# Kernel tuning notes

Measured on AMD Instinct MI355X. Metric: run time of the kernel, lower is better.

The kernel has to match this reference:

```python
import jax, jax.numpy as jnp
import numpy as np

B, H, V, T = 2048, 512, 64, 128

def setup_inputs() -> dict:
    key = jax.random.key(0)
    ks = jax.random.split(key, 7)
    s = 1.0 / np.sqrt(H)
    return {
        "z": jax.random.normal(ks[0], (B, H), dtype=jnp.float32),
        "w_ih": jax.random.uniform(ks[1], (4 * H, H), jnp.float32, -s, s),
        "w_hh": jax.random.uniform(ks[2], (4 * H, H), jnp.float32, -s, s),
        "b_ih": jax.random.uniform(ks[3], (4 * H,), jnp.float32, -s, s),
        "b_hh": jax.random.uniform(ks[4], (4 * H,), jnp.float32, -s, s),
        "fc_w": jax.random.uniform(ks[5], (V, H), jnp.float32, -s, s),
        "fc_b": jax.random.uniform(ks[6], (V,), jnp.float32, -s, s),
    }

def reference(z, w_ih, w_hh, b_ih, b_hh, fc_w, fc_b):
    batch = z.shape[0]
    # Input z is identical at every timestep -> precompute its gate contribution once.
    x_gates = z @ w_ih.T + b_ih + b_hh  # [B, 4H]

    def step(carry, _):
        h, c = carry
        gates = x_gates + h @ w_hh.T  # [B, 4H]
        i, f, g, o = jnp.split(gates, 4, axis=-1)  # PyTorch LSTMCell gate order
        i = jax.nn.sigmoid(i)
        f = jax.nn.sigmoid(f)
        g = jnp.tanh(g)
        o = jax.nn.sigmoid(o)
        c = f * c + i * g
        h = o * jnp.tanh(c)
        return (h, c), h

    h0 = jnp.zeros((batch, w_hh.shape[1]), dtype=z.dtype)
    c0 = jnp.zeros_like(h0)
    _, hs = jax.lax.scan(step, (h0, c0), None, length=T)  # [T, B, H]
    x = jnp.transpose(hs, (1, 0, 2))  # [B, T, H]
    return jax.nn.relu(x @ fc_w.T + fc_b)  # [B, T, V]
```

## Files before the change

kernel.cpp:

```cpp
#include <hip/hip_runtime.h>
#include <hip/hip_bf16.h>
#include <cstdint>

#define B_   2048
#define H_   512
#define T_   128
#define V_   64
#define FOURH 2048

typedef __bf16 bf16x8 __attribute__((ext_vector_type(8)));
typedef float  floatx4 __attribute__((ext_vector_type(4)));
typedef int    intx4   __attribute__((ext_vector_type(4)));

__device__ __forceinline__ unsigned short f2bf(float f) {
    union { float f; uint32_t u; } v; v.f = f;
    uint32_t r = v.u + 0x7fff + ((v.u >> 16) & 1);
    return (unsigned short)(r >> 16);
}

__device__ __forceinline__ float rcp_(float x) {
    float r; asm("v_rcp_f32 %0, %1" : "=v"(r) : "v"(x)); return r;
}
__device__ __forceinline__ float sigmoidf_(float x) {
    return rcp_(1.0f + __expf(-x));
}
__device__ __forceinline__ float tanhf_(float x) {
    float e = __expf(fminf(-2.0f * x, 80.0f));
    return (1.0f - e) * rcp_(1.0f + e);
}

__device__ __forceinline__ void global_to_lds16(const unsigned short* g, unsigned short* l) {
    __builtin_amdgcn_global_load_lds(
        (const __attribute__((address_space(1))) unsigned int*)g,
        (__attribute__((address_space(3))) unsigned int*)l, 16, 0, 0);
}

__device__ __forceinline__ bf16x8 load16_sys(const unsigned short* p) {
    bf16x8 d;
    asm volatile("global_load_dwordx4 %0, %1, off sc0 sc1\n\t"
                 "s_waitcnt vmcnt(0)"
                 : "=v"(d) : "v"(p));
    return d;
}

__device__ __forceinline__ void flag_prefetch(const unsigned int* fp, intx4& f) {
    asm volatile("global_load_dwordx4 %0, %1, off sc0 sc1"
                 : "=v"(f) : "v"(fp) : "memory");
}
__device__ __forceinline__ bool flag_ok(const intx4& f, unsigned int tgt) {
    return (unsigned int)f[0] >= tgt && (unsigned int)f[1] >= tgt &&
           (unsigned int)f[2] >= tgt && (unsigned int)f[3] >= tgt;
}
__device__ __forceinline__ void wait4(const unsigned int* fp, unsigned int tgt) {
    for (;;) {
        intx4 f;
        asm volatile("global_load_dwordx4 %0, %1, off sc0 sc1\n\t"
                     "s_waitcnt vmcnt(0)"
                     : "=v"(f) : "v"(fp) : "memory");
        if (flag_ok(f, tgt)) return;
        __builtin_amdgcn_s_sleep(1);
    }
}
__device__ __forceinline__ void flag_post(unsigned int* p, unsigned int v) {
    asm volatile("global_store_dword %0, %1, off sc0 sc1" :: "v"(p), "v"(v) : "memory");
}

__global__ void prep_kernel(const float* __restrict__ z,
                            const float* __restrict__ w_ih,
                            const float* __restrict__ w_hh,
                            const float* __restrict__ b_ih,
                            const float* __restrict__ b_hh,
                            const float* __restrict__ fc_w,
                            unsigned short* __restrict__ Bp_ih,
                            unsigned short* __restrict__ Bp_hh,
                            unsigned short* __restrict__ z_bf,
                            unsigned short* __restrict__ fcw_bf,
                            float* __restrict__ biasp,
                            unsigned int* __restrict__ cnt) {
    int i = blockIdx.x * blockDim.x + threadIdx.x;
    int col = i >> 9, k = i & 511;
    int jj = col >> 7, cc = col & 127;
    int gate = (cc >> 4) & 3;
    int hcl = ((cc >> 6) << 4) | (cc & 15);
    int p = gate * 512 + jj * 32 + hcl;
    Bp_hh[i] = f2bf(w_hh[p * 512 + k]);
    Bp_ih[i] = f2bf(w_ih[p * 512 + k]);
    z_bf[i]  = f2bf(z[i]);
    if (i < V_ * H_) fcw_bf[i] = f2bf(fc_w[i]);
    if (i < FOURH) {
        int j2 = i >> 7, c2 = i & 127;
        int g2 = (c2 >> 4) & 3;
        int h2 = ((c2 >> 6) << 4) | (c2 & 15);
        int p2 = g2 * 512 + j2 * 32 + h2;
        biasp[i] = b_ih[p2] + b_hh[p2];
    }
    if (i < 1024) cnt[i] = 0;
}

__device__ __forceinline__ void gemm_tile_r1(
        const unsigned short* __restrict__ Aglob,
        const unsigned short* __restrict__ Bglob,
        int arow0, int brow0,
        unsigned short* As, unsigned short* Bs,
        floatx4 acc[2][8], int w, int l) {
    const int lr = l >> 3;
    const int gl = (l & 7) ^ lr;
    const int ln = l & 15, lq = l >> 4, ls = l & 7;
    for (int kc = 0; kc < 8; ++kc) {
        const int kof = kc * 64 + gl * 8;
        #pragma unroll
        for (int q = 0; q < 4; ++q) {
            const int r0 = (w * 4 + q) * 8;
            global_to_lds16(Aglob + (size_t)(arow0 + r0 + lr) * 512 + kof, As + r0 * 64);
            global_to_lds16(Bglob + (size_t)(brow0 + r0 + lr) * 512 + kof, Bs + r0 * 64);
        }
        __syncthreads();
        #pragma unroll
        for (int kk = 0; kk < 2; ++kk) {
            bf16x8 a[2], b[8];
            #pragma unroll
            for (int mt = 0; mt < 2; ++mt) {
                const int m = 32 * w + 16 * mt + ln;
                const int g = kk * 4 + lq;
                a[mt] = *(const bf16x8*)(As + m * 64 + ((g ^ ls) * 8));
            }
            #pragma unroll
            for (int nt = 0; nt < 8; ++nt) {
                const int n = 16 * nt + ln;
                const int g = kk * 4 + lq;
                b[nt] = *(const bf16x8*)(Bs + n * 64 + ((g ^ ls) * 8));
            }
            #pragma unroll
            for (int mt = 0; mt < 2; ++mt)
                #pragma unroll
                for (int nt = 0; nt < 8; ++nt)
                    acc[mt][nt] = __builtin_amdgcn_mfma_f32_16x16x32_bf16(
                        a[mt], b[nt], acc[mt][nt], 0, 0, 0);
        }
        __syncthreads();
    }
}

__global__ void __launch_bounds__(256) xg_gemm_kernel(
        const unsigned short* __restrict__ z_bf,
        const unsigned short* __restrict__ Bp_ih,
        const float* __restrict__ biasp,
        float* __restrict__ xg) {
    __shared__ unsigned short As[128 * 64];
    __shared__ unsigned short Bs[128 * 64];
    const int bi = blockIdx.x, j = blockIdx.y;
    const int tid = threadIdx.x, w = tid >> 6, l = tid & 63;
    floatx4 acc[2][8];
    const floatx4 zf = {0.f, 0.f, 0.f, 0.f};
    for (int a1 = 0; a1 < 2; ++a1) for (int a2 = 0; a2 < 8; ++a2) acc[a1][a2] = zf;

    gemm_tile_r1(z_bf, Bp_ih, bi * 128, j * 128, As, Bs, acc, w, l);

    const int ln = l & 15, lq = l >> 4;
    #pragma unroll
    for (int mt = 0; mt < 2; ++mt)
        #pragma unroll
        for (int nt = 0; nt < 8; ++nt) {
            const int colp = j * 128 + nt * 16 + ln;
            const float bv = biasp[colp];
            #pragma unroll
            for (int r = 0; r < 4; ++r) {
                const int b = bi * 128 + 32 * w + 16 * mt + lq * 4 + r;
                xg[(size_t)b * FOURH + colp] = acc[mt][nt][r] + bv;
            }
        }
}

__device__ __forceinline__ void stage_issue(const unsigned short* __restrict__ Aglob,
                                            int arow0, int kc, int w, int l,
                                            intx4& t0, intx4& t1, intx4& t2, intx4& t3) {
    const int lr = l >> 3;
    const int gl = (l & 7) ^ lr;
    const int kof = kc * 64 + gl * 8;
    const unsigned short* p0 = Aglob + (size_t)(arow0 + (w * 4 + 0) * 8 + lr) * 512 + kof;
    const unsigned short* p1 = Aglob + (size_t)(arow0 + (w * 4 + 1) * 8 + lr) * 512 + kof;
    const unsigned short* p2 = Aglob + (size_t)(arow0 + (w * 4 + 2) * 8 + lr) * 512 + kof;
    const unsigned short* p3 = Aglob + (size_t)(arow0 + (w * 4 + 3) * 8 + lr) * 512 + kof;
    asm volatile(
        "global_load_dwordx4 %0, %4, off sc0 sc1\n\t"
        "global_load_dwordx4 %1, %5, off sc0 sc1\n\t"
        "global_load_dwordx4 %2, %6, off sc0 sc1\n\t"
        "global_load_dwordx4 %3, %7, off sc0 sc1"
        : "=&v"(t0), "=&v"(t1), "=&v"(t2), "=&v"(t3)
        : "v"(p0), "v"(p1), "v"(p2), "v"(p3)
        : "memory");
}

__device__ __forceinline__ void commit8(unsigned short* buf, int w, int l,
                                        const intx4* u) {
    asm volatile("s_waitcnt vmcnt(0)" ::: "memory");
    const int lr = l >> 3, sl = (l & 7) * 8;
    #pragma unroll
    for (int kcL = 0; kcL < 2; ++kcL)
        #pragma unroll
        for (int q = 0; q < 4; ++q)
            *(intx4*)(buf + kcL * 8192 + ((w * 4 + q) * 8 + lr) * 64 + sl) = u[kcL * 4 + q];
}

__global__ void __launch_bounds__(256, 1) lstm_persistent(
        const unsigned short* __restrict__ Bp_hh,
        const unsigned short* __restrict__ fcw_bf,
        const float* __restrict__ xg,
        const float* __restrict__ fc_b,
        unsigned short* __restrict__ h0b,
        unsigned short* __restrict__ h1b,
        unsigned int* __restrict__ cnt,
        float* __restrict__ out) {
    __shared__ unsigned short AsB0[2 * 8192];
    __shared__ unsigned short AsB1[2 * 8192];

    const int bx = blockIdx.x;
    const int bi = bx & 15;
    const int j  = bx >> 4;
    const int tid = threadIdx.x;
    const int w = tid >> 6, l = tid & 63;
    const int wm = w >> 1, wn = w & 1;
    const int ln = l & 15, lq = l >> 4;
    const bool jlt8 = (j < 8);
    const int j16 = j * 16;
    const int v = 16 * w + ln;
    const float fcb_v = fc_b[v];
    const int arow0 = bi * 128;
    unsigned int* flagp = cnt + bi * 64;
    const floatx4 zf = {0.f, 0.f, 0.f, 0.f};

    bf16x8 bq[16][4];
    {
        const unsigned short* bbase =
            Bp_hh + ((size_t)(j * 128 + 64 * wn + ln)) * 512 + lq * 8;
        #pragma unroll
        for (int s = 0; s < 16; ++s)
            #pragma unroll
            for (int nt = 0; nt < 4; ++nt)
                bq[s][nt] = *(const bf16x8*)(bbase + (size_t)nt * 16 * 512 + s * 32);
    }

    floatx4 xga[4][4];
    #pragma unroll
    for (int mt = 0; mt < 4; ++mt)
        #pragma unroll
        for (int nt = 0; nt < 4; ++nt)
            #pragma unroll
            for (int r = 0; r < 4; ++r) {
                const int b = arow0 + 64 * wm + 16 * mt + lq * 4 + r;
                xga[mt][nt][r] = xg[(size_t)b * FOURH + j * 128 + 64 * wn + 16 * nt + ln];
            }

    unsigned short* hlds = AsB0;

    float cst[4][4];
    #pragma unroll
    for (int mt = 0; mt < 4; ++mt)
        #pragma unroll
        for (int r = 0; r < 4; ++r) {
            float iv = sigmoidf_(xga[mt][0][r]);
            float gv = tanhf_  (xga[mt][2][r]);
            float ov = sigmoidf_(xga[mt][3][r]);
            float cv = iv * gv;
            cst[mt][r] = cv;
            hlds[(64 * wm + 16 * mt + lq * 4 + r) * 32 + (wn * 16 + ln)] = f2bf(ov * tanhf_(cv));
        }
    __syncthreads();
    for (int c = tid; c < 512; c += 256) {
        const int row = c >> 2, seg = c & 3;
        intx4 d = *(const intx4*)(hlds + row * 32 + seg * 8);
        const unsigned short* p = h0b + (size_t)(arow0 + row) * 512 + j * 32 + seg * 8;
        asm volatile("global_store_dwordx4 %0, %1, off sc0 sc1" :: "v"(p), "v"(d) : "memory");
    }
    asm volatile("s_waitcnt vmcnt(0)" ::: "memory");
    __syncthreads();
    if (tid == 0) flag_post(flagp + j, 1u);
    intx4 fpre;
    flag_prefetch(flagp, fpre);

    unsigned short* hb[2] = {h0b, h1b};
    #pragma unroll 1
    for (int t = 1; t < T_; ++t) {
        const unsigned int tg = (unsigned int)t;

        asm volatile("s_waitcnt vmcnt(0)" ::: "memory");
        __builtin_amdgcn_sched_barrier(0);
        if (!flag_ok(fpre, tg)) wait4(flagp, tg);

        const unsigned short* hprev = hb[(t - 1) & 1];
        unsigned short* hnext = hb[t & 1];

        floatx4 acc[4][4];
        #pragma unroll
        for (int a1 = 0; a1 < 4; ++a1)
            #pragma unroll
            for (int a2 = 0; a2 < 4; ++a2) acc[a1][a2] = zf;
        floatx4 pacc = zf;

        intx4 u[8];
        stage_issue(hprev, arow0, 0, w, l, u[0], u[1], u[2], u[3]);
        stage_issue(hprev, arow0, 1, w, l, u[4], u[5], u[6], u[7]);
        flag_prefetch(flagp + 4, fpre);
        commit8(AsB0, w, l, u);
        __syncthreads();

        #pragma unroll
        for (int g = 0; g < 4; ++g) {
            if (g < 3) {
                __builtin_amdgcn_sched_barrier(0);
                if (!flag_ok(fpre, tg)) wait4(flagp + 4 * (g + 1), tg);
                stage_issue(hprev, arow0, 2 * g + 2, w, l, u[0], u[1], u[2], u[3]);
                stage_issue(hprev, arow0, 2 * g + 3, w, l, u[4], u[5], u[6], u[7]);
                if (g < 2) flag_prefetch(flagp + 4 * (g + 2), fpre);
            }
            const unsigned short* buf = (g & 1) ? AsB1 : AsB0;
            #pragma unroll
            for (int ss = 0; ss < 4; ++ss) {
                const int s = g * 4 + ss;
                const int ga = (ss & 1) * 4 + lq;
                const unsigned short* Ac = buf + (ss >> 1) * 8192;
                bf16x8 af[4];
                #pragma unroll
                for (int mt = 0; mt < 4; ++mt) {
                    const int m = 64 * wm + 16 * mt + ln;
                    af[mt] = *(const bf16x8*)(Ac + m * 64 + ((ga ^ (ln & 7)) * 8));
                }
                #pragma unroll
                for (int mt = 0; mt < 4; ++mt)
                    #pragma unroll
                    for (int nt = 0; nt < 4; ++nt)
                        acc[mt][nt] = __builtin_amdgcn_mfma_f32_16x16x32_bf16(
                            af[mt], bq[s][nt], acc[mt][nt], 0, 0, 0);
                if (jlt8) {
                    bf16x8 ap = *(const bf16x8*)(Ac + (j16 + ln) * 64 + ((ga ^ (ln & 7)) * 8));
                    bf16x8 bp = *(const bf16x8*)(fcw_bf + (size_t)v * 512 + s * 32 + lq * 8);
                    pacc = __builtin_amdgcn_mfma_f32_16x16x32_bf16(ap, bp, pacc, 0, 0, 0);
                }
            }
            if (g < 3) {
                commit8((g & 1) ? AsB0 : AsB1, w, l, u);
                __syncthreads();
            }
        }

        #pragma unroll
        for (int mt = 0; mt < 4; ++mt)
            #pragma unroll
            for (int r = 0; r < 4; ++r) {
                float iv = sigmoidf_(acc[mt][0][r] + xga[mt][0][r]);
                float fv = sigmoidf_(acc[mt][1][r] + xga[mt][1][r]);
                float gv = tanhf_  (acc[mt][2][r] + xga[mt][2][r]);
                float ov = sigmoidf_(acc[mt][3][r] + xga[mt][3][r]);
                float cn = fv * cst[mt][r] + iv * gv;
                cst[mt][r] = cn;
                hlds[(64 * wm + 16 * mt + lq * 4 + r) * 32 + (wn * 16 + ln)] = f2bf(ov * tanhf_(cn));
            }
        __syncthreads();
        for (int c = tid; c < 512; c += 256) {
            const int row = c >> 2, seg = c & 3;
            intx4 d = *(const intx4*)(hlds + row * 32 + seg * 8);
            const unsigned short* p = hnext + (size_t)(arow0 + row) * 512 + j * 32 + seg * 8;
            asm volatile("global_store_dwordx4 %0, %1, off sc0 sc1" :: "v"(p), "v"(d) : "memory");
        }
        asm volatile("s_waitcnt vmcnt(0)" ::: "memory");
        __syncthreads();
        if (tid == 0) flag_post(flagp + j, tg + 1u);
        flag_prefetch(flagp, fpre);

        if (jlt8) {
            #pragma unroll
            for (int r = 0; r < 4; ++r) {
                const int b = arow0 + j16 + lq * 4 + r;
                out[(size_t)b * (T_ * V_) + (t - 1) * V_ + v] = fmaxf(pacc[r] + fcb_v, 0.0f);
            }
        }
    }

    if (jlt8) {
        wait4(flagp,      T_);
        wait4(flagp + 4,  T_);
        wait4(flagp + 8,  T_);
        wait4(flagp + 12, T_);
        const unsigned short* hlast = hb[(T_ - 1) & 1];
        floatx4 pa = zf;
        const int ar = arow0 + j16 + ln;
        #pragma unroll
        for (int kc = 0; kc < 16; ++kc) {
            const int k = kc * 32 + lq * 8;
            bf16x8 a = load16_sys(hlast + (size_t)ar * 512 + k);
            bf16x8 b = *(const bf16x8*)(fcw_bf + (size_t)v * 512 + k);
            pa = __builtin_amdgcn_mfma_f32_16x16x32_bf16(a, b, pa, 0, 0, 0);
        }
        #pragma unroll
        for (int r = 0; r < 4; ++r) {
            const int b = arow0 + j16 + lq * 4 + r;
            out[(size_t)b * (T_ * V_) + (T_ - 1) * V_ + v] = fmaxf(pa[r] + fcb_v, 0.0f);
        }
    }
}

extern "C" void kernel_launch(void* const* d_in, const int* in_sizes, int n_in,
                              void* d_out, int out_size, void* d_ws, size_t ws_size,
                              hipStream_t stream) {
    const float* z    = (const float*)d_in[0];
    const float* w_ih = (const float*)d_in[1];
    const float* w_hh = (const float*)d_in[2];
    const float* b_ih = (const float*)d_in[3];
    const float* b_hh = (const float*)d_in[4];
    const float* fc_w = (const float*)d_in[5];
    const float* fc_b = (const float*)d_in[6];
    float* out = (float*)d_out;

    char* ws = (char*)d_ws;
    size_t o = 0;
    auto take = [&](size_t bytes) { char* p = ws + o; o += (bytes + 255) & ~(size_t)255; return p; };
    unsigned short* Bp_hh  = (unsigned short*)take((size_t)FOURH * H_ * 2);
    unsigned short* Bp_ih  = (unsigned short*)take((size_t)FOURH * H_ * 2);
    unsigned short* z_bf   = (unsigned short*)take((size_t)B_ * H_ * 2);
    unsigned short* fcw_bf = (unsigned short*)take((size_t)V_ * H_ * 2);
    float*          biasp  = (float*)take((size_t)FOURH * 4);
    unsigned short* hbuf0  = (unsigned short*)take((size_t)B_ * H_ * 2);
    unsigned short* hbuf1  = (unsigned short*)take((size_t)B_ * H_ * 2);
    unsigned int*   cnt    = (unsigned int*)take(16 * 256);
    float*          xg     = (float*)take((size_t)B_ * FOURH * 4);

    prep_kernel<<<(B_ * H_) / 256, 256, 0, stream>>>(z, w_ih, w_hh, b_ih, b_hh, fc_w,
                                                     Bp_ih, Bp_hh, z_bf, fcw_bf, biasp, cnt);
    xg_gemm_kernel<<<dim3(16, 16), 256, 0, stream>>>(z_bf, Bp_ih, biasp, xg);
    lstm_persistent<<<256, 256, 0, stream>>>(Bp_hh, fcw_bf, xg, fc_b,
                                             hbuf0, hbuf1, cnt, out);
}
```

Baseline: 1.567 ms.

## Repartition persistent LSTM grid into 32 batch groups by 8 hidden-column blocks

The persistent LSTM kernel's 256 blocks are re-tiled from 16 batch groups × 16 column slices to 32 batch groups × 8 column slices. Each block now handles 64 batch rows and 256 gate columns, so the shared h tile halves and each block depends on fewer producer flags (8 instead of 16 per group). The aim is to cut per-step h staging traffic and synchronisation fan-in. The trade-off is that each block now holds weight fragments for a 256-wide column slice, and more flag groups are needed.

```diff
diff --git a/kernel.cpp b/kernel.cpp
--- a/kernel.cpp
+++ b/kernel.cpp
@@ -11,6 +11,7 @@
 typedef __bf16 bf16x8 __attribute__((ext_vector_type(8)));
 typedef float  floatx4 __attribute__((ext_vector_type(4)));
 typedef int    intx4   __attribute__((ext_vector_type(4)));
+typedef int    intx2   __attribute__((ext_vector_type(2)));
 
 __device__ __forceinline__ unsigned short f2bf(float f) {
     union { float f; uint32_t u; } v; v.f = f;
@@ -55,9 +56,24 @@
     for (;;) {
         intx4 f;
         asm volatile("global_load_dwordx4 %0, %1, off sc0 sc1\n\t"
-                     "s_waitcnt vmcnt(0)"
-                     : "=v"(f) : "v"(fp) : "memory");
+                     "s_waitcnt vmcnt(0)" : "=v"(f) : "v"(fp) : "memory");
         if (flag_ok(f, tgt)) return;
+        __builtin_amdgcn_s_sleep(1);
+    }
+}
+__device__ __forceinline__ void flag_prefetch2(const unsigned int* fp, intx2& f) {
+    asm volatile("global_load_dwordx2 %0, %1, off sc0 sc1"
+                 : "=v"(f) : "v"(fp) : "memory");
+}
+__device__ __forceinline__ bool flag_ok2(const intx2& f, unsigned int tgt) {
+    return (unsigned int)f[0] >= tgt && (unsigned int)f[1] >= tgt;
+}
+__device__ __forceinline__ void wait2(const unsigned int* fp, unsigned int tgt) {
+    for (;;) {
+        intx2 f;
+        asm volatile("global_load_dwordx2 %0, %1, off sc0 sc1\n\t"
+                     "s_waitcnt vmcnt(0)" : "=v"(f) : "v"(fp) : "memory");
+        if (flag_ok2(f, tgt)) return;
         __builtin_amdgcn_s_sleep(1);
     }
 }
@@ -94,7 +110,7 @@
         int p2 = g2 * 512 + j2 * 32 + h2;
         biasp[i] = b_ih[p2] + b_hh[p2];
     }
-    if (i < 1024) cnt[i] = 0;
+    if (i < 2048) cnt[i] = 0;
 }
 
 __device__ __forceinline__ void gemm_tile_r1(
@@ -171,35 +187,31 @@
         }
 }
 
-__device__ __forceinline__ void stage_issue(const unsigned short* __restrict__ Aglob,
-                                            int arow0, int kc, int w, int l,
-                                            intx4& t0, intx4& t1, intx4& t2, intx4& t3) {
+__device__ __forceinline__ void stage_issue2(const unsigned short* __restrict__ Aglob,
+                                             int arow0, int kc, int w, int l,
+                                             intx4& t0, intx4& t1) {
     const int lr = l >> 3;
     const int gl = (l & 7) ^ lr;
     const int kof = kc * 64 + gl * 8;
-    const unsigned short* p0 = Aglob + (size_t)(arow0 + (w * 4 + 0) * 8 + lr) * 512 + kof;
-    const unsigned short* p1 = Aglob + (size_t)(arow0 + (w * 4 + 1) * 8 + lr) * 512 + kof;
-    const unsigned short* p2 = Aglob + (size_t)(arow0 + (w * 4 + 2) * 8 + lr) * 512 + kof;
-    const unsigned short* p3 = Aglob + (size_t)(arow0 + (w * 4 + 3) * 8 + lr) * 512 + kof;
+    const unsigned short* p0 = Aglob + (size_t)(arow0 + (w * 2 + 0) * 8 + lr) * 512 + kof;
+    const unsigned short* p1 = Aglob + (size_t)(arow0 + (w * 2 + 1) * 8 + lr) * 512 + kof;
     asm volatile(
-        "global_load_dwordx4 %0, %4, off sc0 sc1\n\t"
-        "global_load_dwordx4 %1, %5, off sc0 sc1\n\t"
-        "global_load_dwordx4 %2, %6, off sc0 sc1\n\t"
-        "global_load_dwordx4 %3, %7, off sc0 sc1"
-        : "=&v"(t0), "=&v"(t1), "=&v"(t2), "=&v"(t3)
-        : "v"(p0), "v"(p1), "v"(p2), "v"(p3)
+        "global_load_dwordx4 %0, %2, off sc0 sc1\n\t"
+        "global_load_dwordx4 %1, %3, off sc0 sc1"
+        : "=&v"(t0), "=&v"(t1)
+        : "v"(p0), "v"(p1)
         : "memory");
 }
 
-__device__ __forceinline__ void commit8(unsigned short* buf, int w, int l,
+__device__ __forceinline__ void commit4(unsigned short* buf, int w, int l,
                                         const intx4* u) {
     asm volatile("s_waitcnt vmcnt(0)" ::: "memory");
     const int lr = l >> 3, sl = (l & 7) * 8;
     #pragma unroll
     for (int kcL = 0; kcL < 2; ++kcL)
         #pragma unroll
-        for (int q = 0; q < 4; ++q)
-            *(intx4*)(buf + kcL * 8192 + ((w * 4 + q) * 8 + lr) * 64 + sl) = u[kcL * 4 + q];
+        for (int q = 0; q < 2; ++q)
+            *(intx4*)(buf + kcL * 4096 + ((w * 2 + q) * 8 + lr) * 64 + sl) = u[kcL * 2 + q];
 }
 
 __global__ void __launch_bounds__(256, 1) lstm_persistent(
@@ -211,28 +223,28 @@
         unsigned short* __restrict__ h1b,
         unsigned int* __restrict__ cnt,
         float* __restrict__ out) {
-    __shared__ unsigned short AsB0[2 * 8192];
-    __shared__ unsigned short AsB1[2 * 8192];
+    __shared__ unsigned short AsB0[8192];
+    __shared__ unsigned short AsB1[8192];
 
     const int bx = blockIdx.x;
-    const int bi = bx & 15;
-    const int j  = bx >> 4;
+    const int gi = bx & 31;
+    const int j  = bx >> 5;
     const int tid = threadIdx.x;
     const int w = tid >> 6, l = tid & 63;
-    const int wm = w >> 1, wn = w & 1;
     const int ln = l & 15, lq = l >> 4;
-    const bool jlt8 = (j < 8);
+    const bool jlt4 = (j < 4);
     const int j16 = j * 16;
     const int v = 16 * w + ln;
     const float fcb_v = fc_b[v];
-    const int arow0 = bi * 128;
-    unsigned int* flagp = cnt + bi * 64;
+    const int arow0 = gi * 64;
+    const int colbase = j * 256 + (w >> 1) * 128 + (w & 1) * 64;
+    unsigned int* flagp = cnt + gi * 64;
     const floatx4 zf = {0.f, 0.f, 0.f, 0.f};
 
     bf16x8 bq[16][4];
     {
         const unsigned short* bbase =
-            Bp_hh + ((size_t)(j * 128 + 64 * wn + ln)) * 512 + lq * 8;
+            Bp_hh + ((size_t)(colbase + ln)) * 512 + lq * 8;
         #pragma unroll
         for (int s = 0; s < 16; ++s)
             #pragma unroll
@@ -247,8 +259,8 @@
         for (int nt = 0; nt < 4; ++nt)
             #pragma unroll
             for (int r = 0; r < 4; ++r) {
-                const int b = arow0 + 64 * wm + 16 * mt + lq * 4 + r;
-                xga[mt][nt][r] = xg[(size_t)b * FOURH + j * 128 + 64 * wn + 16 * nt + ln];
+                const int b = arow0 + 16 * mt + lq * 4 + r;
+                xga[mt][nt][r] = xg[(size_t)b * FOURH + colbase + 16 * nt + ln];
             }
 
     unsigned short* hlds = AsB0;
@@ -263,20 +275,20 @@
             float ov = sigmoidf_(xga[mt][3][r]);
             float cv = iv * gv;
             cst[mt][r] = cv;
-            hlds[(64 * wm + 16 * mt + lq * 4 + r) * 32 + (wn * 16 + ln)] = f2bf(ov * tanhf_(cv));
+            hlds[(16 * mt + lq * 4 + r) * 64 + (16 * w + ln)] = f2bf(ov * tanhf_(cv));
         }
     __syncthreads();
     for (int c = tid; c < 512; c += 256) {
-        const int row = c >> 2, seg = c & 3;
-        intx4 d = *(const intx4*)(hlds + row * 32 + seg * 8);
-        const unsigned short* p = h0b + (size_t)(arow0 + row) * 512 + j * 32 + seg * 8;
+        const int row = c >> 3, seg = c & 7;
+        intx4 d = *(const intx4*)(hlds + row * 64 + seg * 8);
+        const unsigned short* p = h0b + (size_t)(arow0 + row) * 512 + j * 64 + seg * 8;
         asm volatile("global_store_dwordx4 %0, %1, off sc0 sc1" :: "v"(p), "v"(d) : "memory");
     }
     asm volatile("s_waitcnt vmcnt(0)" ::: "memory");
     __syncthreads();
     if (tid == 0) flag_post(flagp + j, 1u);
-    intx4 fpre;
-    flag_prefetch(flagp, fpre);
+    intx2 fpre2;
+    flag_prefetch2(flagp, fpre2);
 
     unsigned short* hb[2] = {h0b, h1b};
     #pragma unroll 1
@@ -285,7 +297,7 @@
 
         asm volatile("s_waitcnt vmcnt(0)" ::: "memory");
         __builtin_amdgcn_sched_barrier(0);
-        if (!flag_ok(fpre, tg)) wait4(flagp, tg);
+        if (!flag_ok2(fpre2, tg)) wait2(flagp, tg);
 
         const unsigned short* hprev = hb[(t - 1) & 1];
         unsigned short* hnext = hb[t & 1];
@@ -297,32 +309,32 @@
             for (int a2 = 0; a2 < 4; ++a2) acc[a1][a2] = zf;
         floatx4 pacc = zf;
 
-        intx4 u[8];
-        stage_issue(hprev, arow0, 0, w, l, u[0], u[1], u[2], u[3]);
-        stage_issue(hprev, arow0, 1, w, l, u[4], u[5], u[6], u[7]);
-        flag_prefetch(flagp + 4, fpre);
-        commit8(AsB0, w, l, u);
+        intx4 u[4];
+        stage_issue2(hprev, arow0, 0, w, l, u[0], u[1]);
+        stage_issue2(hprev, arow0, 1, w, l, u[2], u[3]);
+        flag_prefetch2(flagp + 2, fpre2);
+        commit4(AsB0, w, l, u);
         __syncthreads();
 
         #pragma unroll
         for (int g = 0; g < 4; ++g) {
             if (g < 3) {
                 __builtin_amdgcn_sched_barrier(0);
-                if (!flag_ok(fpre, tg)) wait4(flagp + 4 * (g + 1), tg);
-                stage_issue(hprev, arow0, 2 * g + 2, w, l, u[0], u[1], u[2], u[3]);
-                stage_issue(hprev, arow0, 2 * g + 3, w, l, u[4], u[5], u[6], u[7]);
-                if (g < 2) flag_prefetch(flagp + 4 * (g + 2), fpre);
+                if (!flag_ok2(fpre2, tg)) wait2(flagp + 2 * (g + 1), tg);
+                stage_issue2(hprev, arow0, 2 * g + 2, w, l, u[0], u[1]);
+                stage_issue2(hprev, arow0, 2 * g + 3, w, l, u[2], u[3]);
+                if (g < 2) flag_prefetch2(flagp + 2 * (g + 2), fpre2);
             }
             const unsigned short* buf = (g & 1) ? AsB1 : AsB0;
             #pragma unroll
             for (int ss = 0; ss < 4; ++ss) {
                 const int s = g * 4 + ss;
                 const int ga = (ss & 1) * 4 + lq;
-                const unsigned short* Ac = buf + (ss >> 1) * 8192;
+                const unsigned short* Ac = buf + (ss >> 1) * 4096;
                 bf16x8 af[4];
                 #pragma unroll
                 for (int mt = 0; mt < 4; ++mt) {
-                    const int m = 64 * wm + 16 * mt + ln;
+                    const int m = 16 * mt + ln;
                     af[mt] = *(const bf16x8*)(Ac + m * 64 + ((ga ^ (ln & 7)) * 8));
                 }
                 #pragma unroll
@@ -331,14 +343,14 @@
                     for (int nt = 0; nt < 4; ++nt)
                         acc[mt][nt] = __builtin_amdgcn_mfma_f32_16x16x32_bf16(
                             af[mt], bq[s][nt], acc[mt][nt], 0, 0, 0);
-                if (jlt8) {
+                if (jlt4) {
                     bf16x8 ap = *(const bf16x8*)(Ac + (j16 + ln) * 64 + ((ga ^ (ln & 7)) * 8));
                     bf16x8 bp = *(const bf16x8*)(fcw_bf + (size_t)v * 512 + s * 32 + lq * 8);
                     pacc = __builtin_amdgcn_mfma_f32_16x16x32_bf16(ap, bp, pacc, 0, 0, 0);
                 }
             }
             if (g < 3) {
-                commit8((g & 1) ? AsB0 : AsB1, w, l, u);
+                commit4((g & 1) ? AsB0 : AsB1, w, l, u);
                 __syncthreads();
             }
         }
@@ -353,21 +365,21 @@
                 float ov = sigmoidf_(acc[mt][3][r] + xga[mt][3][r]);
                 float cn = fv * cst[mt][r] + iv * gv;
                 cst[mt][r] = cn;
-                hlds[(64 * wm + 16 * mt + lq * 4 + r) * 32 + (wn * 16 + ln)] = f2bf(ov * tanhf_(cn));
+                hlds[(16 * mt + lq * 4 + r) * 64 + (16 * w + ln)] = f2bf(ov * tanhf_(cn));
             }
         __syncthreads();
         for (int c = tid; c < 512; c += 256) {
-            const int row = c >> 2, seg = c & 3;
-            intx4 d = *(const intx4*)(hlds + row * 32 + seg * 8);
-            const unsigned short* p = hnext + (size_t)(arow0 + row) * 512 + j * 32 + seg * 8;
+            const int row = c >> 3, seg = c & 7;
+            intx4 d = *(const intx4*)(hlds + row * 64 + seg * 8);
+            const unsigned short* p = hnext + (size_t)(arow0 + row) * 512 + j * 64 + seg * 8;
             asm volatile("global_store_dwordx4 %0, %1, off sc0 sc1" :: "v"(p), "v"(d) : "memory");
         }
         asm volatile("s_waitcnt vmcnt(0)" ::: "memory");
         __syncthreads();
         if (tid == 0) flag_post(flagp + j, tg + 1u);
-        flag_prefetch(flagp, fpre);
-
-        if (jlt8) {
+        flag_prefetch2(flagp, fpre2);
+
+        if (jlt4) {
             #pragma unroll
             for (int r = 0; r < 4; ++r) {
                 const int b = arow0 + j16 + lq * 4 + r;
@@ -376,11 +388,9 @@
         }
     }
 
-    if (jlt8) {
-        wait4(flagp,      T_);
-        wait4(flagp + 4,  T_);
-        wait4(flagp + 8,  T_);
-        wait4(flagp + 12, T_);
+    if (jlt4) {
+        wait4(flagp,     T_);
+        wait4(flagp + 4, T_);
         const unsigned short* hlast = hb[(T_ - 1) & 1];
         floatx4 pa = zf;
         const int ar = arow0 + j16 + ln;
@@ -421,7 +431,7 @@
     float*          biasp  = (float*)take((size_t)FOURH * 4);
     unsigned short* hbuf0  = (unsigned short*)take((size_t)B_ * H_ * 2);
     unsigned short* hbuf1  = (unsigned short*)take((size_t)B_ * H_ * 2);
-    unsigned int*   cnt    = (unsigned int*)take(16 * 256);
+    unsigned int*   cnt    = (unsigned int*)take(32 * 256);
     float*          xg     = (float*)take((size_t)B_ * FOURH * 4);
 
     prep_kernel<<<(B_ * H_) / 256, 256, 0, stream>>>(z, w_ih, w_hh, b_ih, b_hh, fc_w,
```

Result: no change. 1.563 ms (-0.2%).
